# Kernel tuning notes

Hardware: AMD Instinct MI355X
Metric: run time of the kernel (lower is better)

## Reference

```python
import jax, jax.numpy as jnp
import numpy as np

B, T, NW, NF = 4, 1, 1536, 16
N_CROSS = 400_000
N_EDGES = 1_600_000
C_OUT = 4
IN_DIM = 2 * NF + 2  # 34


def setup_inputs() -> dict:
    key = jax.random.key(0)
    ks = jax.random.split(key, 16)
    return {
        "first_wires": jax.random.normal(ks[0], (B, T, NW, NF), jnp.float32),
        "second_wires": jax.random.normal(ks[1], (B, T, NW, NF), jnp.float32),
        "crossings": jax.random.normal(ks[2], (N_CROSS, 2), jnp.float32),
        "bbox": jax.random.uniform(ks[3], (3,), jnp.float32) + 0.5,
        "edge_attr": jax.random.normal(ks[4], (N_EDGES, 4), jnp.float32),
        "indices": jax.random.randint(ks[5], (N_CROSS, 2), 0, NW),
        "edge_index": jax.random.randint(ks[6], (2, N_EDGES), 0, N_CROSS),
        "W": jax.random.normal(ks[7], (IN_DIM, C_OUT), jnp.float32) / np.sqrt(IN_DIM),
        "att_src": jax.random.normal(ks[8], (C_OUT,), jnp.float32),
        "att_dst": jax.random.normal(ks[9], (C_OUT,), jnp.float32),
        "W_e": jax.random.normal(ks[10], (4, C_OUT), jnp.float32) / 2.0,
        "att_edge": jax.random.normal(ks[11], (C_OUT,), jnp.float32),
        "bias": jnp.zeros((C_OUT,), jnp.float32),
        "w_mlp": jax.random.normal(ks[12], (C_OUT, 1), jnp.float32) / 2.0,
        "b_mlp": jnp.zeros((1,), jnp.float32),
    }


def reference(first_wires, second_wires, crossings, bbox, edge_attr,
              indices, edge_index, W, att_src, att_dst, W_e, att_edge,
              bias, w_mlp, b_mlp):
    b, t = first_wires.shape[0], first_wires.shape[1]
    n = indices.shape[0]
    # fill_window: gather wire features for each crossing and append normalized coords
    fw = first_wires[:, :, indices[:, 0], :]          # [B,T,N,NF]
    sw = second_wires[:, :, indices[:, 1], :]         # [B,T,N,NF]
    xc = crossings / jnp.linalg.norm(bbox)            # [N,2]
    xc = jnp.broadcast_to(xc[None, None], (b, t, n, 2))
    x = jnp.concatenate([fw, sw, xc], axis=-1)        # [B,T,N,2NF+2]
    x = x.reshape(b * t, n, -1)

    src, dst = edge_index[0], edge_index[1]
    h = x @ W                                          # [BT,N,C]
    a_e = (edge_attr @ W_e) @ att_edge                 # [E]

    def gat(hb):
        hs, hd = hb[src], hb[dst]                      # [E,C]
        logits = jax.nn.leaky_relu(hs @ att_src + hd @ att_dst + a_e, 0.2)
        m = jax.ops.segment_max(logits, dst, num_segments=n)
        ex = jnp.exp(logits - m[dst])
        den = jax.ops.segment_sum(ex, dst, num_segments=n)
        alpha = ex / (den[dst] + 1e-16)
        return jax.ops.segment_sum(alpha[:, None] * hs, dst, num_segments=n) + bias

    out = jax.vmap(gat)(h)                             # [BT,N,C]
    y = out @ w_mlp + b_mlp                            # [BT,N,1]
    return y.reshape(b, t, n, 1)
```

## Files before the change

kernel.cpp:

```cpp
#include <hip/hip_runtime.h>
#include <math.h>

#define BB 4
#define NWIRE 1536
#define NFEAT 16
#define BS 256
#define NBLK 256
#define DSHIFT 10
#define MAXNB 512

__global__ void k_wires(const float* __restrict__ fw, const float* __restrict__ sw,
                        const float* __restrict__ W, const float* __restrict__ att_src,
                        const float* __restrict__ att_dst, const float* __restrict__ wmlp,
                        float4* __restrict__ fwpre, float4* __restrict__ swpre) {
    int t = blockIdx.x * blockDim.x + threadIdx.x;
    if (t >= BB * NWIRE) return;
    const float* fp = fw + (size_t)t * NFEAT;
    const float* sp = sw + (size_t)t * NFEAT;
    float hf[4] = {0, 0, 0, 0}, hs[4] = {0, 0, 0, 0};
    #pragma unroll
    for (int k = 0; k < NFEAT; ++k) {
        float a = fp[k], b = sp[k];
        #pragma unroll
        for (int c = 0; c < 4; ++c) {
            hf[c] = fmaf(a, W[k * 4 + c], hf[c]);
            hs[c] = fmaf(b, W[(NFEAT + k) * 4 + c], hs[c]);
        }
    }
    float fs = 0, fd = 0, fq = 0, ss = 0, sd = 0, sq = 0;
    #pragma unroll
    for (int c = 0; c < 4; ++c) {
        float as = att_src[c], ad = att_dst[c], wm = wmlp[c];
        fs = fmaf(hf[c], as, fs); fd = fmaf(hf[c], ad, fd); fq = fmaf(hf[c], wm, fq);
        ss = fmaf(hs[c], as, ss); sd = fmaf(hs[c], ad, sd); sq = fmaf(hs[c], wm, sq);
    }
    fwpre[t] = make_float4(fs, fd, fq, 0.0f);
    swpre[t] = make_float4(ss, sd, sq, 0.0f);
}

__global__ void k_nodes(const int* __restrict__ indices, const float* __restrict__ crossings,
                        const float* __restrict__ bbox, const float* __restrict__ W,
                        const float* __restrict__ att_src, const float* __restrict__ att_dst,
                        const float* __restrict__ wmlp,
                        const float4* __restrict__ fwpre, const float4* __restrict__ swpre,
                        float4* __restrict__ srcdat4, float4* __restrict__ dstdat4, int n) {
    int i = blockIdx.x * blockDim.x + threadIdx.x;
    if (i >= n) return;
    float inv = rsqrtf(bbox[0] * bbox[0] + bbox[1] * bbox[1] + bbox[2] * bbox[2]);
    int i0 = indices[2 * i], i1 = indices[2 * i + 1];
    float x0 = crossings[2 * i] * inv, x1 = crossings[2 * i + 1] * inv;
    float xs = 0, xd = 0, xq = 0;
    #pragma unroll
    for (int c = 0; c < 4; ++c) {
        float hc = fmaf(x0, W[32 * 4 + c], x1 * W[33 * 4 + c]);
        xs = fmaf(hc, att_src[c], xs);
        xd = fmaf(hc, att_dst[c], xd);
        xq = fmaf(hc, wmlp[c], xq);
    }
    float4 f0 = fwpre[0 * NWIRE + i0], s0 = swpre[0 * NWIRE + i1];
    float4 f1 = fwpre[1 * NWIRE + i0], s1 = swpre[1 * NWIRE + i1];
    float4 f2 = fwpre[2 * NWIRE + i0], s2 = swpre[2 * NWIRE + i1];
    float4 f3 = fwpre[3 * NWIRE + i0], s3 = swpre[3 * NWIRE + i1];
    srcdat4[(size_t)i * 2] = make_float4(f0.x + s0.x + xs, f1.x + s1.x + xs,
                                         f2.x + s2.x + xs, f3.x + s3.x + xs);
    srcdat4[(size_t)i * 2 + 1] = make_float4(f0.z + s0.z + xq, f1.z + s1.z + xq,
                                             f2.z + s2.z + xq, f3.z + s3.z + xq);
    dstdat4[i] = make_float4(f0.y + s0.y + xd, f1.y + s1.y + xd,
                             f2.y + s2.y + xd, f3.y + s3.y + xd);
}

__global__ void k_binA1(const int* __restrict__ ei, int ne, int nb, int chunk,
                        int* __restrict__ bh) {
    __shared__ int lc[MAXNB];
    for (int i = threadIdx.x; i < nb; i += BS) lc[i] = 0;
    __syncthreads();
    int blk = blockIdx.x;
    int e0 = blk * chunk, e1 = min(e0 + chunk, ne);
    const int* dstp = ei + ne;
    for (int e = e0 + threadIdx.x; e < e1; e += BS)
        atomicAdd(&lc[dstp[e] >> DSHIFT], 1);
    __syncthreads();
    for (int b = threadIdx.x; b < nb; b += BS)
        bh[b * NBLK + blk] = lc[b];
}

__global__ void k_scanBlk(int* __restrict__ bh, int* __restrict__ btot, int nb) {
    int b = blockIdx.x * blockDim.x + threadIdx.x;
    if (b >= nb) return;
    int4* p = (int4*)(bh + (size_t)b * NBLK);
    int run = 0;
    #pragma unroll 4
    for (int k = 0; k < NBLK / 4; ++k) {
        int4 v = p[k];
        int4 o;
        o.x = run; run += v.x;
        o.y = run; run += v.y;
        o.z = run; run += v.z;
        o.w = run; run += v.w;
        p[k] = o;
    }
    btot[b] = run;
}

__global__ void k_scanBuck(const int* __restrict__ btot, int* __restrict__ bbase,
                           int* __restrict__ start, int nb, int n, int ne) {
    __shared__ int sh[MAXNB];
    int t = threadIdx.x;
    int v = (t < nb) ? btot[t] : 0;
    sh[t] = v;
    __syncthreads();
    for (int ofs = 1; ofs < MAXNB; ofs <<= 1) {
        int u = (t >= ofs) ? sh[t - ofs] : 0;
        __syncthreads();
        sh[t] += u;
        __syncthreads();
    }
    if (t < nb) bbase[t] = sh[t] - v;
    if (t == 0) { bbase[nb] = ne; start[n] = ne; }
}

__global__ void k_binA2(const int* __restrict__ ei, const float* __restrict__ eattr,
                        const float* __restrict__ We, const float* __restrict__ att_edge,
                        const int* __restrict__ bh, const int* __restrict__ bbase,
                        int ne, int nb, int chunk, int2* __restrict__ recs) {
    __shared__ int curs[MAXNB];
    int blk = blockIdx.x;
    for (int b = threadIdx.x; b < nb; b += BS)
        curs[b] = bbase[b] + bh[b * NBLK + blk];
    __syncthreads();
    float v0 = fmaf(We[0], att_edge[0], fmaf(We[1], att_edge[1], fmaf(We[2], att_edge[2], We[3] * att_edge[3])));
    float v1 = fmaf(We[4], att_edge[0], fmaf(We[5], att_edge[1], fmaf(We[6], att_edge[2], We[7] * att_edge[3])));
    float v2 = fmaf(We[8], att_edge[0], fmaf(We[9], att_edge[1], fmaf(We[10], att_edge[2], We[11] * att_edge[3])));
    float v3 = fmaf(We[12], att_edge[0], fmaf(We[13], att_edge[1], fmaf(We[14], att_edge[2], We[15] * att_edge[3])));
    const int* srcp = ei;
    const int* dstp = ei + ne;
    int e0 = blk * chunk, e1 = min(e0 + chunk, ne);
    for (int e = e0 + threadIdx.x; e < e1; e += BS) {
        int s = srcp[e], d = dstp[e];
        const float4 ea = *(const float4*)(eattr + (size_t)e * 4);
        float ae = fmaf(ea.x, v0, fmaf(ea.y, v1, fmaf(ea.z, v2, ea.w * v3)));
        int b = d >> DSHIFT;
        int pos = atomicAdd(&curs[b], 1);
        recs[pos] = make_int2(((d & 1023) << 19) | s, __float_as_int(ae));
    }
}

__global__ void k_binB(const int2* __restrict__ recs, const int* __restrict__ bbase,
                       int2* __restrict__ csr, int* __restrict__ start, int n, int nb) {
    __shared__ int cnt[1024];
    __shared__ int tsum[BS];
    int b = blockIdx.x;
    int r0 = bbase[b], r1 = bbase[b + 1];
    int nrec = r1 - r0;
    for (int i = threadIdx.x; i < 1024; i += BS) cnt[i] = 0;
    __syncthreads();
    for (int i = threadIdx.x; i < nrec; i += BS)
        atomicAdd(&cnt[(unsigned)recs[r0 + i].x >> 19], 1);
    __syncthreads();
    int t = threadIdx.x;
    int c0 = cnt[4 * t], c1 = cnt[4 * t + 1], c2 = cnt[4 * t + 2], c3 = cnt[4 * t + 3];
    int lsum = c0 + c1 + c2 + c3;
    tsum[t] = lsum;
    __syncthreads();
    for (int ofs = 1; ofs < BS; ofs <<= 1) {
        int u = (t >= ofs) ? tsum[t - ofs] : 0;
        __syncthreads();
        tsum[t] += u;
        __syncthreads();
    }
    int base = tsum[t] - lsum;
    cnt[4 * t]     = base;
    cnt[4 * t + 1] = base + c0;
    cnt[4 * t + 2] = base + c0 + c1;
    cnt[4 * t + 3] = base + c0 + c1 + c2;
    __syncthreads();
    int dbase = b << DSHIFT;
    for (int j = threadIdx.x; j < 1024; j += BS) {
        int d = dbase + j;
        if (d < n) start[d] = r0 + cnt[j];
    }
    __syncthreads();
    for (int i = threadIdx.x; i < nrec; i += BS) {
        int2 r = recs[r0 + i];
        int dlo = (unsigned)r.x >> 19;
        int pos = r0 + atomicAdd(&cnt[dlo], 1);
        csr[pos] = make_int2(r.x & 0x7FFFF, r.y);
    }
}

__global__ void k_gat(const int2* __restrict__ csr, const int* __restrict__ start,
                      const float4* __restrict__ srcdat4, const float4* __restrict__ dstdat4,
                      const float* __restrict__ bias, const float* __restrict__ wmlp,
                      const float* __restrict__ bmlp, float* __restrict__ out, int n) {
    int d = blockIdx.x * blockDim.x + threadIdx.x;
    if (d >= n) return;
    int st = start[d], en = start[d + 1];
    float4 pd = dstdat4[d];
    float d0 = 0, d1 = 0, d2 = 0, d3 = 0;
    float n0 = 0, n1 = 0, n2 = 0, n3 = 0;
    for (int j = st; j < en; ++j) {
        int2 r = csr[j];
        float ae = __int_as_float(r.y);
        float4 ps = srcdat4[(size_t)r.x * 2];
        float4 q  = srcdat4[(size_t)r.x * 2 + 1];
        float lg, ex;
        lg = ps.x + pd.x + ae; lg = lg > 0.0f ? lg : 0.2f * lg;
        ex = expf(lg); d0 += ex; n0 = fmaf(ex, q.x, n0);
        lg = ps.y + pd.y + ae; lg = lg > 0.0f ? lg : 0.2f * lg;
        ex = expf(lg); d1 += ex; n1 = fmaf(ex, q.y, n1);
        lg = ps.z + pd.z + ae; lg = lg > 0.0f ? lg : 0.2f * lg;
        ex = expf(lg); d2 += ex; n2 = fmaf(ex, q.z, n2);
        lg = ps.w + pd.w + ae; lg = lg > 0.0f ? lg : 0.2f * lg;
        ex = expf(lg); d3 += ex; n3 = fmaf(ex, q.w, n3);
    }
    float cst = fmaf(bias[0], wmlp[0], fmaf(bias[1], wmlp[1], fmaf(bias[2], wmlp[2], bias[3] * wmlp[3]))) + bmlp[0];
    out[d]                 = n0 / (d0 + 1e-16f) + cst;
    out[(size_t)n + d]     = n1 / (d1 + 1e-16f) + cst;
    out[(size_t)2 * n + d] = n2 / (d2 + 1e-16f) + cst;
    out[(size_t)3 * n + d] = n3 / (d3 + 1e-16f) + cst;
}

extern "C" void kernel_launch(void* const* d_in, const int* in_sizes, int n_in,
                              void* d_out, int out_size, void* d_ws, size_t ws_size,
                              hipStream_t stream) {
    const float* first_wires  = (const float*)d_in[0];
    const float* second_wires = (const float*)d_in[1];
    const float* crossings    = (const float*)d_in[2];
    const float* bbox         = (const float*)d_in[3];
    const float* edge_attr    = (const float*)d_in[4];
    const int*   indices      = (const int*)d_in[5];
    const int*   edge_index   = (const int*)d_in[6];
    const float* W            = (const float*)d_in[7];
    const float* att_src      = (const float*)d_in[8];
    const float* att_dst      = (const float*)d_in[9];
    const float* W_e          = (const float*)d_in[10];
    const float* att_edge     = (const float*)d_in[11];
    const float* bias         = (const float*)d_in[12];
    const float* w_mlp        = (const float*)d_in[13];
    const float* b_mlp        = (const float*)d_in[14];
    float* out = (float*)d_out;

    const int n  = in_sizes[5] / 2;
    const int ne = in_sizes[6] / 2;
    const int nb = (n + 1023) >> DSHIFT;
    const int chunk = (ne + NBLK - 1) / NBLK;

    char* ws = (char*)d_ws;
    size_t off = 0;
    float4* fwpre   = (float4*)(ws + off); off += (size_t)BB * NWIRE * 16;
    float4* swpre   = (float4*)(ws + off); off += (size_t)BB * NWIRE * 16;
    float4* srcdat4 = (float4*)(ws + off); off += (size_t)n * 32;
    float4* dstdat4 = (float4*)(ws + off); off += (size_t)n * 16;
    int*    bh      = (int*)(ws + off);    off += (size_t)nb * NBLK * 4;
    int*    btot    = (int*)(ws + off);    off += ((size_t)nb * 4 + 15) & ~15ull;
    int*    bbase   = (int*)(ws + off);    off += ((size_t)(nb + 1) * 4 + 15) & ~15ull;
    int*    start   = (int*)(ws + off);    off += ((size_t)(n + 1) * 4 + 15) & ~15ull;
    int2*   recs    = (int2*)(ws + off);   off += (size_t)ne * 8;
    int2*   csr     = (int2*)(ws + off);   off += (size_t)ne * 8;

    hipLaunchKernelGGL(k_wires, dim3((BB * NWIRE + BS - 1) / BS), dim3(BS), 0, stream,
                       first_wires, second_wires, W, att_src, att_dst, w_mlp, fwpre, swpre);
    hipLaunchKernelGGL(k_nodes, dim3((n + BS - 1) / BS), dim3(BS), 0, stream,
                       indices, crossings, bbox, W, att_src, att_dst, w_mlp,
                       fwpre, swpre, srcdat4, dstdat4, n);
    hipLaunchKernelGGL(k_binA1, dim3(NBLK), dim3(BS), 0, stream,
                       edge_index, ne, nb, chunk, bh);
    hipLaunchKernelGGL(k_scanBlk, dim3((nb + 63) / 64), dim3(64), 0, stream,
                       bh, btot, nb);
    hipLaunchKernelGGL(k_scanBuck, dim3(1), dim3(MAXNB), 0, stream,
                       btot, bbase, start, nb, n, ne);
    hipLaunchKernelGGL(k_binA2, dim3(NBLK), dim3(BS), 0, stream,
                       edge_index, edge_attr, W_e, att_edge, bh, bbase, ne, nb, chunk, recs);
    hipLaunchKernelGGL(k_binB, dim3(nb), dim3(BS), 0, stream,
                       recs, bbase, csr, start, n, nb);
    hipLaunchKernelGGL(k_gat, dim3((n + BS - 1) / BS), dim3(BS), 0, stream,
                       csr, start, srcdat4, dstdat4, bias, w_mlp, b_mlp, out, n);
}
```

Before: 227.8 us.

## Fuse second binning pass into GAT via shared-memory atomic accumulation per bucket

Drops the per-destination CSR sort kernel and the per-destination GAT kernel. A single kernel now walks each bucket's records, computes the attention terms, and accumulates numerator and denominator in shared memory with float atomics. Bucket width is halved to 512 destinations to fit the shared accumulators, which doubles the bucket count and the k_scanBuck block size. This removes a full read and write of the edge records and one launch, at the cost of contended LDS float atomics and non-deterministic summation order.

```diff
diff --git a/kernel.cpp b/kernel.cpp
--- a/kernel.cpp
+++ b/kernel.cpp
@@ -6,8 +6,9 @@
 #define NFEAT 16
 #define BS 256
 #define NBLK 256
-#define DSHIFT 10
-#define MAXNB 512
+#define DSHIFT 9
+#define DPB (1 << DSHIFT)
+#define MAXNB 1024
 
 __global__ void k_wires(const float* __restrict__ fw, const float* __restrict__ sw,
                         const float* __restrict__ W, const float* __restrict__ att_src,
@@ -103,7 +104,7 @@
 }
 
 __global__ void k_scanBuck(const int* __restrict__ btot, int* __restrict__ bbase,
-                           int* __restrict__ start, int nb, int n, int ne) {
+                           int nb, int ne) {
     __shared__ int sh[MAXNB];
     int t = threadIdx.x;
     int v = (t < nb) ? btot[t] : 0;
@@ -116,7 +117,7 @@
         __syncthreads();
     }
     if (t < nb) bbase[t] = sh[t] - v;
-    if (t == 0) { bbase[nb] = ne; start[n] = ne; }
+    if (t == 0) bbase[nb] = ne;
 }
 
 __global__ void k_binA2(const int* __restrict__ ei, const float* __restrict__ eattr,
@@ -141,83 +142,55 @@
         float ae = fmaf(ea.x, v0, fmaf(ea.y, v1, fmaf(ea.z, v2, ea.w * v3)));
         int b = d >> DSHIFT;
         int pos = atomicAdd(&curs[b], 1);
-        recs[pos] = make_int2(((d & 1023) << 19) | s, __float_as_int(ae));
-    }
-}
-
-__global__ void k_binB(const int2* __restrict__ recs, const int* __restrict__ bbase,
-                       int2* __restrict__ csr, int* __restrict__ start, int n, int nb) {
-    __shared__ int cnt[1024];
-    __shared__ int tsum[BS];
+        recs[pos] = make_int2(((d & (DPB - 1)) << 19) | s, __float_as_int(ae));
+    }
+}
+
+__global__ void k_gatB(const int2* __restrict__ recs, const int* __restrict__ bbase,
+                       const float4* __restrict__ srcdat4, const float4* __restrict__ dstdat4,
+                       const float* __restrict__ bias, const float* __restrict__ wmlp,
+                       const float* __restrict__ bmlp, float* __restrict__ out, int n) {
+    __shared__ float acc[DPB * 8];
+    __shared__ float pds[DPB * 4];
     int b = blockIdx.x;
     int r0 = bbase[b], r1 = bbase[b + 1];
-    int nrec = r1 - r0;
-    for (int i = threadIdx.x; i < 1024; i += BS) cnt[i] = 0;
-    __syncthreads();
-    for (int i = threadIdx.x; i < nrec; i += BS)
-        atomicAdd(&cnt[(unsigned)recs[r0 + i].x >> 19], 1);
-    __syncthreads();
-    int t = threadIdx.x;
-    int c0 = cnt[4 * t], c1 = cnt[4 * t + 1], c2 = cnt[4 * t + 2], c3 = cnt[4 * t + 3];
-    int lsum = c0 + c1 + c2 + c3;
-    tsum[t] = lsum;
-    __syncthreads();
-    for (int ofs = 1; ofs < BS; ofs <<= 1) {
-        int u = (t >= ofs) ? tsum[t - ofs] : 0;
-        __syncthreads();
-        tsum[t] += u;
-        __syncthreads();
-    }
-    int base = tsum[t] - lsum;
-    cnt[4 * t]     = base;
-    cnt[4 * t + 1] = base + c0;
-    cnt[4 * t + 2] = base + c0 + c1;
-    cnt[4 * t + 3] = base + c0 + c1 + c2;
-    __syncthreads();
     int dbase = b << DSHIFT;
-    for (int j = threadIdx.x; j < 1024; j += BS) {
-        int d = dbase + j;
-        if (d < n) start[d] = r0 + cnt[j];
-    }
-    __syncthreads();
-    for (int i = threadIdx.x; i < nrec; i += BS) {
-        int2 r = recs[r0 + i];
+    int dmax = min(DPB, n - dbase);
+    for (int i = threadIdx.x; i < DPB * 8; i += BS) acc[i] = 0.0f;
+    for (int i = threadIdx.x; i < dmax; i += BS) {
+        float4 pd = dstdat4[dbase + i];
+        pds[i * 4]     = pd.x;
+        pds[i * 4 + 1] = pd.y;
+        pds[i * 4 + 2] = pd.z;
+        pds[i * 4 + 3] = pd.w;
+    }
+    __syncthreads();
+    for (int i = r0 + threadIdx.x; i < r1; i += BS) {
+        int2 r = recs[i];
         int dlo = (unsigned)r.x >> 19;
-        int pos = r0 + atomicAdd(&cnt[dlo], 1);
-        csr[pos] = make_int2(r.x & 0x7FFFF, r.y);
-    }
-}
-
-__global__ void k_gat(const int2* __restrict__ csr, const int* __restrict__ start,
-                      const float4* __restrict__ srcdat4, const float4* __restrict__ dstdat4,
-                      const float* __restrict__ bias, const float* __restrict__ wmlp,
-                      const float* __restrict__ bmlp, float* __restrict__ out, int n) {
-    int d = blockIdx.x * blockDim.x + threadIdx.x;
-    if (d >= n) return;
-    int st = start[d], en = start[d + 1];
-    float4 pd = dstdat4[d];
-    float d0 = 0, d1 = 0, d2 = 0, d3 = 0;
-    float n0 = 0, n1 = 0, n2 = 0, n3 = 0;
-    for (int j = st; j < en; ++j) {
-        int2 r = csr[j];
+        int src = r.x & 0x7FFFF;
         float ae = __int_as_float(r.y);
-        float4 ps = srcdat4[(size_t)r.x * 2];
-        float4 q  = srcdat4[(size_t)r.x * 2 + 1];
+        float4 ps = srcdat4[(size_t)src * 2];
+        float4 q  = srcdat4[(size_t)src * 2 + 1];
         float lg, ex;
-        lg = ps.x + pd.x + ae; lg = lg > 0.0f ? lg : 0.2f * lg;
-        ex = expf(lg); d0 += ex; n0 = fmaf(ex, q.x, n0);
-        lg = ps.y + pd.y + ae; lg = lg > 0.0f ? lg : 0.2f * lg;
-        ex = expf(lg); d1 += ex; n1 = fmaf(ex, q.y, n1);
-        lg = ps.z + pd.z + ae; lg = lg > 0.0f ? lg : 0.2f * lg;
-        ex = expf(lg); d2 += ex; n2 = fmaf(ex, q.z, n2);
-        lg = ps.w + pd.w + ae; lg = lg > 0.0f ? lg : 0.2f * lg;
-        ex = expf(lg); d3 += ex; n3 = fmaf(ex, q.w, n3);
-    }
+        lg = ps.x + pds[dlo * 4]     + ae; lg = lg > 0.0f ? lg : 0.2f * lg; ex = expf(lg);
+        atomicAdd(&acc[dlo * 8],     ex); atomicAdd(&acc[dlo * 8 + 1], ex * q.x);
+        lg = ps.y + pds[dlo * 4 + 1] + ae; lg = lg > 0.0f ? lg : 0.2f * lg; ex = expf(lg);
+        atomicAdd(&acc[dlo * 8 + 2], ex); atomicAdd(&acc[dlo * 8 + 3], ex * q.y);
+        lg = ps.z + pds[dlo * 4 + 2] + ae; lg = lg > 0.0f ? lg : 0.2f * lg; ex = expf(lg);
+        atomicAdd(&acc[dlo * 8 + 4], ex); atomicAdd(&acc[dlo * 8 + 5], ex * q.z);
+        lg = ps.w + pds[dlo * 4 + 3] + ae; lg = lg > 0.0f ? lg : 0.2f * lg; ex = expf(lg);
+        atomicAdd(&acc[dlo * 8 + 6], ex); atomicAdd(&acc[dlo * 8 + 7], ex * q.w);
+    }
+    __syncthreads();
     float cst = fmaf(bias[0], wmlp[0], fmaf(bias[1], wmlp[1], fmaf(bias[2], wmlp[2], bias[3] * wmlp[3]))) + bmlp[0];
-    out[d]                 = n0 / (d0 + 1e-16f) + cst;
-    out[(size_t)n + d]     = n1 / (d1 + 1e-16f) + cst;
-    out[(size_t)2 * n + d] = n2 / (d2 + 1e-16f) + cst;
-    out[(size_t)3 * n + d] = n3 / (d3 + 1e-16f) + cst;
+    for (int i = threadIdx.x; i < dmax; i += BS) {
+        int d = dbase + i;
+        out[d]                 = acc[i * 8 + 1] / (acc[i * 8]     + 1e-16f) + cst;
+        out[(size_t)n + d]     = acc[i * 8 + 3] / (acc[i * 8 + 2] + 1e-16f) + cst;
+        out[(size_t)2 * n + d] = acc[i * 8 + 5] / (acc[i * 8 + 4] + 1e-16f) + cst;
+        out[(size_t)3 * n + d] = acc[i * 8 + 7] / (acc[i * 8 + 6] + 1e-16f) + cst;
+    }
 }
 
 extern "C" void kernel_launch(void* const* d_in, const int* in_sizes, int n_in,
@@ -242,7 +215,7 @@
 
     const int n  = in_sizes[5] / 2;
     const int ne = in_sizes[6] / 2;
-    const int nb = (n + 1023) >> DSHIFT;
+    const int nb = (n + DPB - 1) >> DSHIFT;
     const int chunk = (ne + NBLK - 1) / NBLK;
 
     char* ws = (char*)d_ws;
@@ -254,9 +227,7 @@
     int*    bh      = (int*)(ws + off);    off += (size_t)nb * NBLK * 4;
     int*    btot    = (int*)(ws + off);    off += ((size_t)nb * 4 + 15) & ~15ull;
     int*    bbase   = (int*)(ws + off);    off += ((size_t)(nb + 1) * 4 + 15) & ~15ull;
-    int*    start   = (int*)(ws + off);    off += ((size_t)(n + 1) * 4 + 15) & ~15ull;
     int2*   recs    = (int2*)(ws + off);   off += (size_t)ne * 8;
-    int2*   csr     = (int2*)(ws + off);   off += (size_t)ne * 8;
 
     hipLaunchKernelGGL(k_wires, dim3((BB * NWIRE + BS - 1) / BS), dim3(BS), 0, stream,
                        first_wires, second_wires, W, att_src, att_dst, w_mlp, fwpre, swpre);
@@ -268,11 +239,9 @@
     hipLaunchKernelGGL(k_scanBlk, dim3((nb + 63) / 64), dim3(64), 0, stream,
                        bh, btot, nb);
     hipLaunchKernelGGL(k_scanBuck, dim3(1), dim3(MAXNB), 0, stream,
-                       btot, bbase, start, nb, n, ne);
+                       btot, bbase, nb, ne);
     hipLaunchKernelGGL(k_binA2, dim3(NBLK), dim3(BS), 0, stream,
                        edge_index, edge_attr, W_e, att_edge, bh, bbase, ne, nb, chunk, recs);
-    hipLaunchKernelGGL(k_binB, dim3(nb), dim3(BS), 0, stream,
-                       recs, bbase, csr, start, n, nb);
-    hipLaunchKernelGGL(k_gat, dim3((n + BS - 1) / BS), dim3(BS), 0, stream,
-                       csr, start, srcdat4, dstdat4, bias, w_mlp, b_mlp, out, n);
-}
+    hipLaunchKernelGGL(k_gatB, dim3(nb), dim3(BS), 0, stream,
+                       recs, bbase, srcdat4, dstdat4, bias, w_mlp, b_mlp, out, n);
+}
```

Result: slower. 264.5 us (+16.1%).
